# Kernel optimization log

Hardware: AMD Instinct MI355X
Metric: run time of the kernel (lower is better)

Reference implementation:

```python
import jax, jax.numpy as jnp
import numpy as np

N_NODES = 100000
N_EDGES = 3200000
IN_C, HID, OUT_C = 128, 256, 128
N_GRAPHS = 64
EPS = 1e-5


def setup_inputs() -> dict:
    key = jax.random.key(0)
    ks = jax.random.split(key, 16)
    x = jax.random.normal(ks[0], (N_NODES, IN_C), dtype=jnp.float32)
    edge_index = jax.random.randint(ks[1], (2, N_EDGES), 0, N_NODES, dtype=jnp.int64 if jax.config.jax_enable_x64 else jnp.int32)
    batch = jnp.sort(jax.random.randint(ks[2], (N_NODES,), 0, N_GRAPHS, dtype=jnp.int32))
    def glorot(k, shape):
        lim = jnp.sqrt(6.0 / (shape[-2] + shape[-1]))
        return jax.random.uniform(k, shape, jnp.float32, -lim, lim)
    return {
        "x": x,
        "W_in": glorot(ks[3], (IN_C, HID)),
        "b_in": jnp.zeros((HID,), jnp.float32),
        "g_in": jnp.ones((HID,), jnp.float32),
        "be_in": jnp.zeros((HID,), jnp.float32),
        "W_hid": glorot(ks[4], (2, HID, HID)),
        "b_hid": jnp.zeros((2, HID), jnp.float32),
        "g_hid": jnp.ones((2, HID), jnp.float32),
        "be_hid": jnp.zeros((2, HID), jnp.float32),
        "W_out": glorot(ks[5], (HID, OUT_C)),
        "b_out": jnp.zeros((OUT_C,), jnp.float32),
        "g_out": jnp.ones((OUT_C,), jnp.float32),
        "be_out": jnp.zeros((OUT_C,), jnp.float32),
        "edge_index": edge_index,
        "batch": batch,
    }


def _gcn_norm(edge_index, n_nodes):
    # add self-loops, symmetric deg^-1/2 normalization (PyG GCNConv defaults)
    loop = jnp.arange(n_nodes, dtype=edge_index.dtype)
    src = jnp.concatenate([edge_index[0], loop])
    dst = jnp.concatenate([edge_index[1], loop])
    deg = jax.ops.segment_sum(jnp.ones_like(dst, dtype=jnp.float32), dst, num_segments=n_nodes)
    dinv = jnp.where(deg > 0, jax.lax.rsqrt(deg), 0.0)
    norm = dinv[src] * dinv[dst]  # [E+N]
    return src, dst, norm


def _block(x, W, b, g, be, src, dst, norm, n_nodes):
    h = x @ W  # [N, out]
    agg = jax.ops.segment_sum(h[src] * norm[:, None], dst, num_segments=n_nodes) + b
    a = jax.nn.leaky_relu(agg, negative_slope=0.01)
    mu = jnp.mean(a, axis=0)
    var = jnp.mean(jnp.square(a - mu), axis=0)
    return (a - mu) * jax.lax.rsqrt(var + EPS) * g + be


def reference(x, W_in, b_in, g_in, be_in, W_hid, b_hid, g_hid, be_hid,
              W_out, b_out, g_out, be_out, edge_index, batch):
    n = x.shape[0]
    src, dst, norm = _gcn_norm(edge_index, n)
    h = _block(x, W_in, b_in, g_in, be_in, src, dst, norm, n)
    for i in range(W_hid.shape[0]):
        h = _block(h, W_hid[i], b_hid[i], g_hid[i], be_hid[i], src, dst, norm, n)
    h = _block(h, W_out, b_out, g_out, be_out, src, dst, norm, n)
    # global mean pool over graphs
    sums = jax.ops.segment_sum(h, batch, num_segments=N_GRAPHS)
    cnts = jax.ops.segment_sum(jnp.ones((n,), h.dtype), batch, num_segments=N_GRAPHS)
    return sums / jnp.maximum(cnts, 1.0)[:, None]
```

## Files before the change

### kernel.cpp

```cpp
#include <hip/hip_runtime.h>
#include <stdint.h>

#define EPS_LN 1e-5f

typedef short bf16x8 __attribute__((ext_vector_type(8)));
typedef float f32x4  __attribute__((ext_vector_type(4)));

__device__ __forceinline__ unsigned short f2bf(float f) {
    unsigned u = __float_as_uint(f);
    unsigned r = (u + 0x7fffu + ((u >> 16) & 1u)) >> 16;
    return (unsigned short)r;
}
__device__ __forceinline__ float bf_lo(unsigned u) { return __uint_as_float(u << 16); }
__device__ __forceinline__ float bf_hi(unsigned u) { return __uint_as_float(u & 0xffff0000u); }

__device__ __forceinline__ void async16(void* lds, const void* g) {
    __builtin_amdgcn_global_load_lds(
        (const __attribute__((address_space(1))) unsigned int*)g,
        (__attribute__((address_space(3))) unsigned int*)lds, 16, 0, 0);
}


__global__ void count_deg_kernel(const int* __restrict__ dst, int E, unsigned* __restrict__ deg) {
    int e = blockIdx.x * blockDim.x + threadIdx.x;
    if (e < E) atomicAdd(&deg[dst[e]], 1u);
}

__global__ void dinv_kernel(const unsigned* __restrict__ deg, float* __restrict__ dinv, int N) {
    int i = blockIdx.x * blockDim.x + threadIdx.x;
    if (i < N) dinv[i] = rsqrtf((float)(deg[i] + 1u));
}

__global__ void block_sums_kernel(const unsigned* __restrict__ deg, unsigned* __restrict__ part, int N) {
    __shared__ unsigned s[256];
    int t = threadIdx.x;
    int i0 = blockIdx.x * 512 + t * 2;
    unsigned a = (i0 < N) ? deg[i0] : 0u;
    unsigned b = (i0 + 1 < N) ? deg[i0 + 1] : 0u;
    s[t] = a + b;
    __syncthreads();
    for (int off = 128; off > 0; off >>= 1) {
        if (t < off) s[t] += s[t + off];
        __syncthreads();
    }
    if (t == 0) part[blockIdx.x] = s[0];
}

__global__ void scan_part_kernel(unsigned* __restrict__ part, unsigned* __restrict__ row_ptr,
                                 int NB, int N) {
    __shared__ unsigned s[256];
    int t = threadIdx.x;
    unsigned v = (t < NB) ? part[t] : 0u;
    s[t] = v;
    __syncthreads();
    for (int off = 1; off < 256; off <<= 1) {
        unsigned u = (t >= off) ? s[t - off] : 0u;
        __syncthreads();
        s[t] += u;
        __syncthreads();
    }
    if (t < NB) part[t] = s[t] - v;
    if (t == 255) row_ptr[N] = s[255];
}

__global__ void scan_blocks_kernel(const unsigned* __restrict__ deg, const unsigned* __restrict__ part,
                                   unsigned* __restrict__ row_ptr, unsigned* __restrict__ cursor, int N) {
    __shared__ unsigned s[256];
    int t = threadIdx.x;
    int i0 = blockIdx.x * 512 + t * 2;
    unsigned a = (i0 < N) ? deg[i0] : 0u;
    unsigned b = (i0 + 1 < N) ? deg[i0 + 1] : 0u;
    unsigned pair = a + b;
    s[t] = pair;
    __syncthreads();
    for (int off = 1; off < 256; off <<= 1) {
        unsigned u = (t >= off) ? s[t - off] : 0u;
        __syncthreads();
        s[t] += u;
        __syncthreads();
    }
    unsigned excl = s[t] - pair + part[blockIdx.x];
    if (i0 < N)     { row_ptr[i0] = excl;         cursor[i0] = excl; }
    if (i0 + 1 < N) { row_ptr[i0 + 1] = excl + a; cursor[i0 + 1] = excl + a; }
}

__global__ void fill_csr_kernel(const int* __restrict__ src, const int* __restrict__ dst,
                                const float* __restrict__ dinv, int E,
                                unsigned* __restrict__ cursor, uint2* __restrict__ csr) {
    int e = blockIdx.x * blockDim.x + threadIdx.x;
    if (e < E) {
        int d = dst[e];
        int s = src[e];
        unsigned pos = atomicAdd(&cursor[d], 1u);
        float w = dinv[d] * dinv[s];
        csr[pos] = make_uint2((unsigned)s, __float_as_uint(w));
    }
}

__global__ void cvt_bf_kernel(const float* __restrict__ in, unsigned* __restrict__ out, int n2) {
    int i = blockIdx.x * blockDim.x + threadIdx.x;
    if (i < n2) {
        float2 v = *reinterpret_cast<const float2*>(&in[(size_t)i * 2]);
        out[i] = (unsigned)f2bf(v.x) | ((unsigned)f2bf(v.y) << 16);
    }
}

__global__ void prep_wt_kernel(const float* __restrict__ W, unsigned short* __restrict__ Wt,
                               int K, int NN) {
    int idx = blockIdx.x * blockDim.x + threadIdx.x;
    if (idx < K * NN) {
        int k = idx / NN, c = idx % NN;
        Wt[(size_t)c * K + k] = f2bf(W[idx]);
    }
}

__global__ void prep_wout_kernel(const float* __restrict__ W, const float* __restrict__ s_arr,
                                 unsigned short* __restrict__ Wt) {
    int idx = blockIdx.x * blockDim.x + threadIdx.x;
    if (idx < 256 * 128) {
        int k = idx >> 7, c = idx & 127;
        Wt[(size_t)c * 256 + k] = f2bf(s_arr[k] * W[idx]);
    }
}

__global__ void tw_kernel(const float* __restrict__ W, const float* __restrict__ t_arr,
                          float* __restrict__ tW) {
    int c = threadIdx.x;
    float acc = 0.f;
    for (int k = 0; k < 256; ++k) acc += t_arr[k] * W[k * 128 + c];
    tW[c] = acc;
}

template<int VEC, bool AFF, bool FINAL>
__global__ void aggregate_bf(const unsigned* __restrict__ X, void* __restrict__ outp,
                             const unsigned* __restrict__ row_ptr, const uint2* __restrict__ csr,
                             const float* __restrict__ dinv,
                             const float* __restrict__ s_aff, const float* __restrict__ t_aff,
                             const float* __restrict__ tW, const float* __restrict__ bias, int N) {
    const unsigned RSU = VEC * 32;
    int node = blockIdx.x * 4 + (threadIdx.x >> 6);
    if (node >= N) return;
    node = __builtin_amdgcn_readfirstlane(node);
    int lane = threadIdx.x & 63;
    unsigned cu = (unsigned)lane * (VEC / 2);

    float di = dinv[node];
    float w0 = di * di;
    float acc[VEC];
    float wsum = w0;
    {
        const unsigned* xr = X + (size_t)((unsigned)node * RSU + cu);
        if constexpr (VEC == 4) {
            uint2 v = *reinterpret_cast<const uint2*>(xr);
            acc[0] = w0 * bf_lo(v.x); acc[1] = w0 * bf_hi(v.x);
            acc[2] = w0 * bf_lo(v.y); acc[3] = w0 * bf_hi(v.y);
        } else {
            unsigned v = *xr;
            acc[0] = w0 * bf_lo(v); acc[1] = w0 * bf_hi(v);
        }
    }
    unsigned e0 = __builtin_amdgcn_readfirstlane(row_ptr[node]);
    unsigned e1 = __builtin_amdgcn_readfirstlane(row_ptr[node + 1]);
    unsigned cnt = e1 - e0;
    unsigned full = cnt & ~7u;

    if constexpr (VEC == 4) {
        for (unsigned i = 0; i < full; i += 8) {
            uint2 p[8];
            #pragma unroll
            for (int u = 0; u < 8; ++u) p[u] = csr[e0 + i + u];
            uint2 v[8];
            #pragma unroll
            for (int u = 0; u < 8; ++u)
                v[u] = *reinterpret_cast<const uint2*>(X + (size_t)(p[u].x * RSU + cu));
            #pragma unroll
            for (int u = 0; u < 8; ++u) {
                float f = __uint_as_float(p[u].y);
                acc[0] += f * bf_lo(v[u].x); acc[1] += f * bf_hi(v[u].x);
                acc[2] += f * bf_lo(v[u].y); acc[3] += f * bf_hi(v[u].y);
                wsum += f;
            }
        }
        for (unsigned i = full; i < cnt; ++i) {
            uint2 p = csr[e0 + i];
            uint2 v = *reinterpret_cast<const uint2*>(X + (size_t)(p.x * RSU + cu));
            float f = __uint_as_float(p.y);
            acc[0] += f * bf_lo(v.x); acc[1] += f * bf_hi(v.x);
            acc[2] += f * bf_lo(v.y); acc[3] += f * bf_hi(v.y);
            wsum += f;
        }
    } else {
        for (unsigned i = 0; i < full; i += 8) {
            uint2 p[8];
            #pragma unroll
            for (int u = 0; u < 8; ++u) p[u] = csr[e0 + i + u];
            unsigned v[8];
            #pragma unroll
            for (int u = 0; u < 8; ++u) v[u] = X[(size_t)(p[u].x * RSU + cu)];
            #pragma unroll
            for (int u = 0; u < 8; ++u) {
                float f = __uint_as_float(p[u].y);
                acc[0] += f * bf_lo(v[u]); acc[1] += f * bf_hi(v[u]);
                wsum += f;
            }
        }
        for (unsigned i = full; i < cnt; ++i) {
            uint2 p = csr[e0 + i];
            unsigned v = X[(size_t)(p.x * RSU + cu)];
            float f = __uint_as_float(p.y);
            acc[0] += f * bf_lo(v); acc[1] += f * bf_hi(v);
            wsum += f;
        }
    }

    int col = lane * VEC;
    float z[VEC];
    #pragma unroll
    for (int j = 0; j < VEC; ++j) {
        float f = acc[j];
        if constexpr (AFF) f = s_aff[col + j] * f + t_aff[col + j] * wsum;
        if constexpr (FINAL) {
            f = f + wsum * tW[col + j] + bias[col + j];
            f = f > 0.f ? f : 0.01f * f;
        }
        z[j] = f;
    }
    if constexpr (FINAL) {
        float* of = (float*)outp;
        *reinterpret_cast<float2*>(&of[(size_t)node * (VEC * 64) + col]) = make_float2(z[0], z[1]);
    } else {
        unsigned* ou = (unsigned*)outp;
        if constexpr (VEC == 4) {
            uint2 p;
            p.x = (unsigned)f2bf(z[0]) | ((unsigned)f2bf(z[1]) << 16);
            p.y = (unsigned)f2bf(z[2]) | ((unsigned)f2bf(z[3]) << 16);
            *reinterpret_cast<uint2*>(&ou[(size_t)((unsigned)node * RSU + cu)]) = p;
        } else {
            ou[(size_t)((unsigned)node * RSU + cu)] = (unsigned)f2bf(z[0]) | ((unsigned)f2bf(z[1]) << 16);
        }
    }
}

template<int K, int NN, bool EPI>
__launch_bounds__(256)
__global__ void gemm_mfma(const unsigned short* __restrict__ Z, const unsigned short* __restrict__ Wt,
                          const float* __restrict__ bias, unsigned short* __restrict__ out,
                          float* __restrict__ stat_sum, float* __restrict__ stat_sq, int M) {
    __shared__ char smem[32768];
    __shared__ float csum[128], csq[128];

    const int tid = threadIdx.x;
    const int lane = tid & 63;
    const int w = tid >> 6;
    const int wr = (w >> 1) * 64;
    const int wc = (w & 1) * 64;
    const int rowBase = blockIdx.x * 128;
    const int colBase = blockIdx.y * 128;
    const int frow = lane & 15;
    const int kgrp = lane >> 4;

    f32x4 acc[4][4] = {};

    for (int kt = 0; kt < K / 64; ++kt) {
        #pragma unroll
        for (int i = 0; i < 4; ++i) {
            int g = (i * 4 + w) * 64 + lane;
            int r = g >> 3;
            int bl = (g & 7) * 16;
            int bg = bl ^ ((r & 7) << 4);
            const char* src = (const char*)Z + (((size_t)(rowBase + r) * K + kt * 64) << 1) + bg;
            async16(&smem[(i * 4 + w) * 1024], src);
        }
        #pragma unroll
        for (int i = 0; i < 4; ++i) {
            int g = (i * 4 + w) * 64 + lane;
            int r = g >> 3;
            int bl = (g & 7) * 16;
            int bg = bl ^ ((r & 7) << 4);
            const char* src = (const char*)Wt + (((size_t)(colBase + r) * K + kt * 64) << 1) + bg;
            async16(&smem[16384 + (i * 4 + w) * 1024], src);
        }
        __syncthreads();
        #pragma unroll
        for (int kk = 0; kk < 2; ++kk) {
            const int kbyte = kk * 64 + kgrp * 16;
            bf16x8 af[4], bfr[4];
            #pragma unroll
            for (int m = 0; m < 4; ++m) {
                int r = wr + m * 16 + frow;
                af[m] = *reinterpret_cast<const bf16x8*>(&smem[r * 128 + (kbyte ^ ((r & 7) << 4))]);
            }
            #pragma unroll
            for (int n = 0; n < 4; ++n) {
                int c = wc + n * 16 + frow;
                bfr[n] = *reinterpret_cast<const bf16x8*>(&smem[16384 + c * 128 + (kbyte ^ ((c & 7) << 4))]);
            }
            #pragma unroll
            for (int m = 0; m < 4; ++m)
                #pragma unroll
                for (int n = 0; n < 4; ++n)
                    acc[m][n] = __builtin_amdgcn_mfma_f32_16x16x32_bf16(bfr[n], af[m], acc[m][n], 0, 0, 0);
        }
        __syncthreads();
    }

    if constexpr (EPI) {
        if (tid < 128) { csum[tid] = 0.f; csq[tid] = 0.f; }
        __syncthreads();
    }

    #pragma unroll
    for (int n = 0; n < 4; ++n) {
        const int c_local = wc + n * 16 + kgrp * 4;
        const int col = colBase + c_local;
        float4 b4 = make_float4(0.f, 0.f, 0.f, 0.f);
        if constexpr (EPI) b4 = *reinterpret_cast<const float4*>(&bias[col]);
        float ps[4] = {0.f, 0.f, 0.f, 0.f}, pq[4] = {0.f, 0.f, 0.f, 0.f};
        #pragma unroll
        for (int m = 0; m < 4; ++m) {
            int row = rowBase + wr + m * 16 + frow;
            if (row < M) {
                float f0 = acc[m][n][0] + b4.x;
                float f1 = acc[m][n][1] + b4.y;
                float f2 = acc[m][n][2] + b4.z;
                float f3 = acc[m][n][3] + b4.w;
                if constexpr (EPI) {
                    f0 = f0 > 0.f ? f0 : 0.01f * f0;
                    f1 = f1 > 0.f ? f1 : 0.01f * f1;
                    f2 = f2 > 0.f ? f2 : 0.01f * f2;
                    f3 = f3 > 0.f ? f3 : 0.01f * f3;
                }
                uint2 pk;
                pk.x = (unsigned)f2bf(f0) | ((unsigned)f2bf(f1) << 16);
                pk.y = (unsigned)f2bf(f2) | ((unsigned)f2bf(f3) << 16);
                *reinterpret_cast<uint2*>(&out[(size_t)row * NN + col]) = pk;
                if constexpr (EPI) {
                    ps[0] += f0; ps[1] += f1; ps[2] += f2; ps[3] += f3;
                    pq[0] += f0 * f0; pq[1] += f1 * f1; pq[2] += f2 * f2; pq[3] += f3 * f3;
                }
            }
        }
        if constexpr (EPI) {
            #pragma unroll
            for (int s = 1; s < 16; s <<= 1) {
                #pragma unroll
                for (int j = 0; j < 4; ++j) {
                    ps[j] += __shfl_xor(ps[j], s);
                    pq[j] += __shfl_xor(pq[j], s);
                }
            }
            if (frow == 0) {
                #pragma unroll
                for (int j = 0; j < 4; ++j) {
                    atomicAdd(&csum[c_local + j], ps[j]);
                    atomicAdd(&csq[c_local + j], pq[j]);
                }
            }
        }
    }
    if constexpr (EPI) {
        __syncthreads();
        if (tid < 128) {
            atomicAdd(&stat_sum[colBase + tid], csum[tid]);
            atomicAdd(&stat_sq[colBase + tid], csq[tid]);
        }
    }
}

__global__ void finalize_kernel(const float* __restrict__ g, const float* __restrict__ be,
                                float* __restrict__ stat_sum, float* __restrict__ stat_sq,
                                float* __restrict__ s_arr, float* __restrict__ t_arr,
                                int C, float invN) {
    int i = threadIdx.x;
    if (i < C) {
        float mu = stat_sum[i] * invN;
        float var = stat_sq[i] * invN - mu * mu;
        float rs = rsqrtf(var + EPS_LN);
        float s = g[i] * rs;
        s_arr[i] = s;
        t_arr[i] = be[i] - mu * s;
        stat_sum[i] = 0.f;
        stat_sq[i] = 0.f;
    }
}

__global__ void stats_pool_kernel(const float* __restrict__ A, const int* __restrict__ batch,
                                  float* __restrict__ stat_sum, float* __restrict__ stat_sq,
                                  float* __restrict__ psums, float* __restrict__ pcnt, int N) {
    int c = threadIdx.x;
    int n0 = blockIdx.x * 256;
    if (n0 >= N) return;
    int n1 = min(n0 + 256, N);
    float cs = 0.f, cq = 0.f;
    float acc = 0.f, cacc = 0.f;
    int curg = -1;
    for (int n = n0; n < n1; ++n) {
        float v = A[(size_t)n * 128 + c];
        cs += v; cq += v * v;
        int g = batch[n];
        if (g != curg) {
            if (curg >= 0) {
                atomicAdd(&psums[curg * 128 + c], acc);
                if (c == 0) atomicAdd(&pcnt[curg], cacc);
            }
            acc = 0.f; cacc = 0.f; curg = g;
        }
        acc += v;
        cacc += 1.f;
    }
    if (curg >= 0) {
        atomicAdd(&psums[curg * 128 + c], acc);
        if (c == 0) atomicAdd(&pcnt[curg], cacc);
    }
    atomicAdd(&stat_sum[c], cs);
    atomicAdd(&stat_sq[c], cq);
}

__global__ void divide_kernel(const float* __restrict__ psums, const float* __restrict__ pcnt,
                              const float* __restrict__ s_arr, const float* __restrict__ t_arr,
                              float* __restrict__ out) {
    int i = blockIdx.x * blockDim.x + threadIdx.x;
    if (i < 64 * 128) {
        int g = i >> 7, c = i & 127;
        float cnt = pcnt[g];
        out[i] = (cnt > 0.f) ? s_arr[c] * (psums[i] / cnt) + t_arr[c] : 0.f;
    }
}

extern "C" void kernel_launch(void* const* d_in, const int* in_sizes, int n_in,
                              void* d_out, int out_size, void* d_ws, size_t ws_size,
                              hipStream_t stream) {
    const float* x      = (const float*)d_in[0];
    const float* W_in   = (const float*)d_in[1];
    const float* b_in   = (const float*)d_in[2];
    const float* g_in   = (const float*)d_in[3];
    const float* be_in  = (const float*)d_in[4];
    const float* W_hid  = (const float*)d_in[5];
    const float* b_hid  = (const float*)d_in[6];
    const float* g_hid  = (const float*)d_in[7];
    const float* be_hid = (const float*)d_in[8];
    const float* W_out  = (const float*)d_in[9];
    const float* b_out  = (const float*)d_in[10];
    const float* g_out  = (const float*)d_in[11];
    const float* be_out = (const float*)d_in[12];
    const int*   eidx   = (const int*)d_in[13];
    const int*   batch  = (const int*)d_in[14];
    float* out = (float*)d_out;

    const int N = in_sizes[14];
    const int E = in_sizes[13] / 2;
    const int Npad = ((N + 127) / 128) * 128;
    const int NB = (N + 511) / 512;
    const int* e_src = eidx;
    const int* e_dst = eidx + E;

    char* ws = (char*)d_ws;
    size_t off = 0;
    auto alloc = [&](size_t bytes) -> void* {
        void* p = ws + off;
        off = (off + bytes + 255) & ~(size_t)255;
        return p;
    };
    char* B1 = (char*)alloc((size_t)Npad * 256 * 2);
    char* B2 = (char*)alloc((size_t)Npad * 256 * 2);
    unsigned* deg      = (unsigned*)alloc((size_t)N * 4);
    float*    dinv     = (float*)alloc((size_t)N * 4);
    unsigned* row_ptr  = (unsigned*)alloc((size_t)(N + 1) * 4);
    unsigned* cursor   = (unsigned*)alloc((size_t)N * 4);
    unsigned* part     = (unsigned*)alloc(256 * 4);
    uint2*    csr      = (uint2*)alloc((size_t)E * 8);
    unsigned short* Wt_in  = (unsigned short*)alloc(256 * 128 * 2);
    unsigned short* Wt_h0  = (unsigned short*)alloc(256 * 256 * 2);
    unsigned short* Wt_h1  = (unsigned short*)alloc(256 * 256 * 2);
    unsigned short* Wt_out = (unsigned short*)alloc(128 * 256 * 2);
    float*    tW       = (float*)alloc(128 * 4);
    float*    stat_sum = (float*)alloc(256 * 4);
    float*    stat_sq  = (float*)alloc(256 * 4);
    float*    s_arr    = (float*)alloc(256 * 4);
    float*    t_arr    = (float*)alloc(256 * 4);
    float*    psums    = (float*)alloc(64 * 128 * 4);
    float*    pcnt     = (float*)alloc(64 * 4);

    const float invN = 1.0f / (float)N;

    hipMemsetAsync(deg, 0, (size_t)N * 4, stream);
    hipMemsetAsync(stat_sum, 0, 256 * 4, stream);
    hipMemsetAsync(stat_sq, 0, 256 * 4, stream);
    hipMemsetAsync(psums, 0, 64 * 128 * 4, stream);
    hipMemsetAsync(pcnt, 0, 64 * 4, stream);

    int egrid = (E + 255) / 256;
    count_deg_kernel<<<egrid, 256, 0, stream>>>(e_dst, E, deg);
    dinv_kernel<<<(N + 255) / 256, 256, 0, stream>>>(deg, dinv, N);
    block_sums_kernel<<<NB, 256, 0, stream>>>(deg, part, N);
    scan_part_kernel<<<1, 256, 0, stream>>>(part, row_ptr, NB, N);
    scan_blocks_kernel<<<NB, 256, 0, stream>>>(deg, part, row_ptr, cursor, N);
    fill_csr_kernel<<<egrid, 256, 0, stream>>>(e_src, e_dst, dinv, E, cursor, csr);

    cvt_bf_kernel<<<(N * 64 + 255) / 256, 256, 0, stream>>>(x, (unsigned*)B2, N * 64);
    prep_wt_kernel<<<(128 * 256 + 255) / 256, 256, 0, stream>>>(W_in, Wt_in, 128, 256);
    prep_wt_kernel<<<(256 * 256 + 255) / 256, 256, 0, stream>>>(W_hid, Wt_h0, 256, 256);
    prep_wt_kernel<<<(256 * 256 + 255) / 256, 256, 0, stream>>>(W_hid + 65536, Wt_h1, 256, 256);

    const int aggGrid = (N + 3) / 4;
    dim3 gg256(Npad / 128, 2);
    dim3 gg128(Npad / 128, 1);

    aggregate_bf<2, false, false><<<aggGrid, 256, 0, stream>>>(
        (const unsigned*)B2, B1, row_ptr, csr, dinv, nullptr, nullptr, nullptr, nullptr, N);
    gemm_mfma<128, 256, true><<<gg256, 256, 0, stream>>>(
        (const unsigned short*)B1, Wt_in, b_in, (unsigned short*)B2, stat_sum, stat_sq, N);
    finalize_kernel<<<1, 256, 0, stream>>>(g_in, be_in, stat_sum, stat_sq, s_arr, t_arr, 256, invN);

    aggregate_bf<4, true, false><<<aggGrid, 256, 0, stream>>>(
        (const unsigned*)B2, B1, row_ptr, csr, dinv, s_arr, t_arr, nullptr, nullptr, N);
    gemm_mfma<256, 256, true><<<gg256, 256, 0, stream>>>(
        (const unsigned short*)B1, Wt_h0, b_hid, (unsigned short*)B2, stat_sum, stat_sq, N);
    finalize_kernel<<<1, 256, 0, stream>>>(g_hid, be_hid, stat_sum, stat_sq, s_arr, t_arr, 256, invN);

    aggregate_bf<4, true, false><<<aggGrid, 256, 0, stream>>>(
        (const unsigned*)B2, B1, row_ptr, csr, dinv, s_arr, t_arr, nullptr, nullptr, N);
    gemm_mfma<256, 256, true><<<gg256, 256, 0, stream>>>(
        (const unsigned short*)B1, Wt_h1, b_hid + 256, (unsigned short*)B2, stat_sum, stat_sq, N);
    finalize_kernel<<<1, 256, 0, stream>>>(g_hid + 256, be_hid + 256, stat_sum, stat_sq, s_arr, t_arr, 256, invN);

    prep_wout_kernel<<<(256 * 128 + 255) / 256, 256, 0, stream>>>(W_out, s_arr, Wt_out);
    tw_kernel<<<1, 128, 0, stream>>>(W_out, t_arr, tW);
    gemm_mfma<256, 128, false><<<gg128, 256, 0, stream>>>(
        (const unsigned short*)B2, Wt_out, nullptr, (unsigned short*)B1, nullptr, nullptr, N);
    aggregate_bf<2, false, true><<<aggGrid, 256, 0, stream>>>(
        (const unsigned*)B1, B2, row_ptr, csr, dinv, nullptr, nullptr, tW, b_out, N);

    stats_pool_kernel<<<(N + 255) / 256, 128, 0, stream>>>(
        (const float*)B2, batch, stat_sum, stat_sq, psums, pcnt, N);
    finalize_kernel<<<1, 256, 0, stream>>>(g_out, be_out, stat_sum, stat_sq, s_arr, t_arr, 128, invN);
    divide_kernel<<<(64 * 128 + 255) / 256, 256, 0, stream>>>(psums, pcnt, s_arr, t_arr, out);
}
```

Measured before the change: 1.292 ms.

## Fuse neighbor aggregation with MFMA GEMM and BN stats per layer

Adds a fused kernel where each wave aggregates 16 nodes' neighbor rows into registers, applies the affine BN transform, stores the bf16 rows to LDS, and multiplies them by the weight matrix with MFMA. Bias, leaky-relu and statistics accumulation happen in the epilogue. This removes the intermediate aggregated buffer round-trip and separate launches for the first three layers. Each node is now handled by 4 lanes with a serial edge loop, which gives less unrolled gather parallelism than the previous per-node wave design. Unused VEC=4 paths in the aggregate kernel are removed.

```diff
diff --git a/kernel.cpp b/kernel.cpp
--- a/kernel.cpp
+++ b/kernel.cpp
@@ -131,6 +131,179 @@
     tW[c] = acc;
 }
 
+template<int K, int NN, bool AFF>
+__launch_bounds__(256)
+__global__ void fused_layer(const unsigned* __restrict__ in, const unsigned short* __restrict__ Wt,
+                            const float* __restrict__ bias,
+                            const float* __restrict__ s_aff, const float* __restrict__ t_aff,
+                            unsigned short* __restrict__ out,
+                            const unsigned* __restrict__ row_ptr, const uint2* __restrict__ csr,
+                            const float* __restrict__ dinv,
+                            float* __restrict__ stat_sum, float* __restrict__ stat_sq, int N) {
+    constexpr int COLS = K / 4;
+    constexpr int NU   = K / 8;
+    constexpr int NL4  = NU / 4;
+    constexpr int NF   = NN / 16;
+
+    __shared__ char alds[4 * 16 * K * 2];
+    __shared__ float csum[NN], csq[NN];
+
+    const int tid = threadIdx.x;
+    const int lane = tid & 63;
+    const int w = tid >> 6;
+
+    for (int i = tid; i < NN; i += 256) { csum[i] = 0.f; csq[i] = 0.f; }
+    __syncthreads();
+
+    const int nq = lane >> 2;
+    const int part = lane & 3;
+    const int rowBase = blockIdx.x * 64 + w * 16;
+    const int node = rowBase + nq;
+
+    float acc[COLS];
+    #pragma unroll
+    for (int i = 0; i < COLS; ++i) acc[i] = 0.f;
+    float wsum = 0.f;
+    unsigned e0 = 0, e1 = 0;
+
+    if (node < N) {
+        float di = dinv[node];
+        float w0 = di * di;
+        const unsigned* bp = in + (size_t)node * (K / 2) + part * NU;
+        uint4 v[NL4];
+        #pragma unroll
+        for (int i = 0; i < NL4; ++i) v[i] = *reinterpret_cast<const uint4*>(bp + i * 4);
+        #pragma unroll
+        for (int i = 0; i < NL4; ++i) {
+            unsigned uu[4] = {v[i].x, v[i].y, v[i].z, v[i].w};
+            #pragma unroll
+            for (int q = 0; q < 4; ++q) {
+                acc[i * 8 + q * 2 + 0] = w0 * bf_lo(uu[q]);
+                acc[i * 8 + q * 2 + 1] = w0 * bf_hi(uu[q]);
+            }
+        }
+        wsum = w0;
+        e0 = row_ptr[node];
+        e1 = row_ptr[node + 1];
+    }
+
+    for (unsigned e = e0; e < e1; ++e) {
+        uint2 p = csr[e];
+        float f = __uint_as_float(p.y);
+        const unsigned* bp = in + (size_t)p.x * (K / 2) + part * NU;
+        uint4 v[NL4];
+        #pragma unroll
+        for (int i = 0; i < NL4; ++i) v[i] = *reinterpret_cast<const uint4*>(bp + i * 4);
+        #pragma unroll
+        for (int i = 0; i < NL4; ++i) {
+            unsigned uu[4] = {v[i].x, v[i].y, v[i].z, v[i].w};
+            #pragma unroll
+            for (int q = 0; q < 4; ++q) {
+                acc[i * 8 + q * 2 + 0] += f * bf_lo(uu[q]);
+                acc[i * 8 + q * 2 + 1] += f * bf_hi(uu[q]);
+            }
+        }
+        wsum += f;
+    }
+
+    if constexpr (AFF) {
+        #pragma unroll
+        for (int i = 0; i < COLS / 4; ++i) {
+            int c = part * COLS + i * 4;
+            float4 s4 = *reinterpret_cast<const float4*>(&s_aff[c]);
+            float4 t4 = *reinterpret_cast<const float4*>(&t_aff[c]);
+            acc[i * 4 + 0] = s4.x * acc[i * 4 + 0] + t4.x * wsum;
+            acc[i * 4 + 1] = s4.y * acc[i * 4 + 1] + t4.y * wsum;
+            acc[i * 4 + 2] = s4.z * acc[i * 4 + 2] + t4.z * wsum;
+            acc[i * 4 + 3] = s4.w * acc[i * 4 + 3] + t4.w * wsum;
+        }
+    }
+
+    {
+        char* myrow = alds + w * (16 * K * 2) + nq * (K * 2);
+        #pragma unroll
+        for (int i = 0; i < NL4; ++i) {
+            uint4 pk;
+            pk.x = (unsigned)f2bf(acc[i * 8 + 0]) | ((unsigned)f2bf(acc[i * 8 + 1]) << 16);
+            pk.y = (unsigned)f2bf(acc[i * 8 + 2]) | ((unsigned)f2bf(acc[i * 8 + 3]) << 16);
+            pk.z = (unsigned)f2bf(acc[i * 8 + 4]) | ((unsigned)f2bf(acc[i * 8 + 5]) << 16);
+            pk.w = (unsigned)f2bf(acc[i * 8 + 6]) | ((unsigned)f2bf(acc[i * 8 + 7]) << 16);
+            int off = (part * (NU * 4) + i * 16) ^ ((nq & 7) << 4);
+            *reinterpret_cast<uint4*>(myrow + off) = pk;
+        }
+    }
+
+    const int frow = lane & 15;
+    const int kgrp = lane >> 4;
+    f32x4 macc[NF] = {};
+    const char* wbase = alds + w * (16 * K * 2);
+
+    #pragma unroll
+    for (int kt = 0; kt < K / 32; ++kt) {
+        int aoff = frow * (K * 2) + ((kt * 64 + kgrp * 16) ^ ((frow & 7) << 4));
+        bf16x8 af = *reinterpret_cast<const bf16x8*>(wbase + aoff);
+        #pragma unroll
+        for (int g = 0; g < NF / 4; ++g) {
+            bf16x8 bf0 = *reinterpret_cast<const bf16x8*>(Wt + ((size_t)((g * 4 + 0) * 16 + frow)) * K + kt * 32 + kgrp * 8);
+            bf16x8 bf1 = *reinterpret_cast<const bf16x8*>(Wt + ((size_t)((g * 4 + 1) * 16 + frow)) * K + kt * 32 + kgrp * 8);
+            bf16x8 bf2 = *reinterpret_cast<const bf16x8*>(Wt + ((size_t)((g * 4 + 2) * 16 + frow)) * K + kt * 32 + kgrp * 8);
+            bf16x8 bf3 = *reinterpret_cast<const bf16x8*>(Wt + ((size_t)((g * 4 + 3) * 16 + frow)) * K + kt * 32 + kgrp * 8);
+            macc[g * 4 + 0] = __builtin_amdgcn_mfma_f32_16x16x32_bf16(bf0, af, macc[g * 4 + 0], 0, 0, 0);
+            macc[g * 4 + 1] = __builtin_amdgcn_mfma_f32_16x16x32_bf16(bf1, af, macc[g * 4 + 1], 0, 0, 0);
+            macc[g * 4 + 2] = __builtin_amdgcn_mfma_f32_16x16x32_bf16(bf2, af, macc[g * 4 + 2], 0, 0, 0);
+            macc[g * 4 + 3] = __builtin_amdgcn_mfma_f32_16x16x32_bf16(bf3, af, macc[g * 4 + 3], 0, 0, 0);
+        }
+    }
+
+    const int orow = rowBase + frow;
+    const bool rok = orow < N;
+    #pragma unroll
+    for (int n = 0; n < NF; ++n) {
+        const int c0 = n * 16 + kgrp * 4;
+        float4 b4 = *reinterpret_cast<const float4*>(&bias[c0]);
+        float f0 = macc[n][0] + b4.x;
+        float f1 = macc[n][1] + b4.y;
+        float f2 = macc[n][2] + b4.z;
+        float f3 = macc[n][3] + b4.w;
+        f0 = f0 > 0.f ? f0 : 0.01f * f0;
+        f1 = f1 > 0.f ? f1 : 0.01f * f1;
+        f2 = f2 > 0.f ? f2 : 0.01f * f2;
+        f3 = f3 > 0.f ? f3 : 0.01f * f3;
+        float ps[4], pq[4];
+        if (rok) {
+            uint2 pk;
+            pk.x = (unsigned)f2bf(f0) | ((unsigned)f2bf(f1) << 16);
+            pk.y = (unsigned)f2bf(f2) | ((unsigned)f2bf(f3) << 16);
+            *reinterpret_cast<uint2*>(&out[(size_t)orow * NN + c0]) = pk;
+            ps[0] = f0; ps[1] = f1; ps[2] = f2; ps[3] = f3;
+            pq[0] = f0 * f0; pq[1] = f1 * f1; pq[2] = f2 * f2; pq[3] = f3 * f3;
+        } else {
+            ps[0] = ps[1] = ps[2] = ps[3] = 0.f;
+            pq[0] = pq[1] = pq[2] = pq[3] = 0.f;
+        }
+        #pragma unroll
+        for (int s = 1; s < 16; s <<= 1) {
+            #pragma unroll
+            for (int j = 0; j < 4; ++j) {
+                ps[j] += __shfl_xor(ps[j], s);
+                pq[j] += __shfl_xor(pq[j], s);
+            }
+        }
+        if (frow == 0) {
+            #pragma unroll
+            for (int j = 0; j < 4; ++j) {
+                atomicAdd(&csum[c0 + j], ps[j]);
+                atomicAdd(&csq[c0 + j], pq[j]);
+            }
+        }
+    }
+    __syncthreads();
+    for (int i = tid; i < NN; i += 256) {
+        atomicAdd(&stat_sum[i], csum[i]);
+        atomicAdd(&stat_sq[i], csq[i]);
+    }
+}
+
 template<int VEC, bool AFF, bool FINAL>
 __global__ void aggregate_bf(const unsigned* __restrict__ X, void* __restrict__ outp,
                              const unsigned* __restrict__ row_ptr, const uint2* __restrict__ csr,
@@ -150,67 +323,34 @@
     float wsum = w0;
     {
         const unsigned* xr = X + (size_t)((unsigned)node * RSU + cu);
-        if constexpr (VEC == 4) {
-            uint2 v = *reinterpret_cast<const uint2*>(xr);
-            acc[0] = w0 * bf_lo(v.x); acc[1] = w0 * bf_hi(v.x);
-            acc[2] = w0 * bf_lo(v.y); acc[3] = w0 * bf_hi(v.y);
-        } else {
-            unsigned v = *xr;
-            acc[0] = w0 * bf_lo(v); acc[1] = w0 * bf_hi(v);
-        }
+        unsigned v = *xr;
+        acc[0] = w0 * bf_lo(v); acc[1] = w0 * bf_hi(v);
     }
     unsigned e0 = __builtin_amdgcn_readfirstlane(row_ptr[node]);
     unsigned e1 = __builtin_amdgcn_readfirstlane(row_ptr[node + 1]);
     unsigned cnt = e1 - e0;
     unsigned full = cnt & ~7u;
 
-    if constexpr (VEC == 4) {
-        for (unsigned i = 0; i < full; i += 8) {
-            uint2 p[8];
-            #pragma unroll
-            for (int u = 0; u < 8; ++u) p[u] = csr[e0 + i + u];
-            uint2 v[8];
-            #pragma unroll
-            for (int u = 0; u < 8; ++u)
-                v[u] = *reinterpret_cast<const uint2*>(X + (size_t)(p[u].x * RSU + cu));
-            #pragma unroll
-            for (int u = 0; u < 8; ++u) {
-                float f = __uint_as_float(p[u].y);
-                acc[0] += f * bf_lo(v[u].x); acc[1] += f * bf_hi(v[u].x);
-                acc[2] += f * bf_lo(v[u].y); acc[3] += f * bf_hi(v[u].y);
-                wsum += f;
-            }
-        }
-        for (unsigned i = full; i < cnt; ++i) {
-            uint2 p = csr[e0 + i];
-            uint2 v = *reinterpret_cast<const uint2*>(X + (size_t)(p.x * RSU + cu));
-            float f = __uint_as_float(p.y);
-            acc[0] += f * bf_lo(v.x); acc[1] += f * bf_hi(v.x);
-            acc[2] += f * bf_lo(v.y); acc[3] += f * bf_hi(v.y);
+    for (unsigned i = 0; i < full; i += 8) {
+        uint2 p[8];
+        #pragma unroll
+        for (int u = 0; u < 8; ++u) p[u] = csr[e0 + i + u];
+        unsigned v[8];
+        #pragma unroll
+        for (int u = 0; u < 8; ++u) v[u] = X[(size_t)(p[u].x * RSU + cu)];
+        #pragma unroll
+        for (int u = 0; u < 8; ++u) {
+            float f = __uint_as_float(p[u].y);
+            acc[0] += f * bf_lo(v[u]); acc[1] += f * bf_hi(v[u]);
             wsum += f;
         }
-    } else {
-        for (unsigned i = 0; i < full; i += 8) {
-            uint2 p[8];
-            #pragma unroll
-            for (int u = 0; u < 8; ++u) p[u] = csr[e0 + i + u];
-            unsigned v[8];
-            #pragma unroll
-            for (int u = 0; u < 8; ++u) v[u] = X[(size_t)(p[u].x * RSU + cu)];
-            #pragma unroll
-            for (int u = 0; u < 8; ++u) {
-                float f = __uint_as_float(p[u].y);
-                acc[0] += f * bf_lo(v[u]); acc[1] += f * bf_hi(v[u]);
-                wsum += f;
-            }
-        }
-        for (unsigned i = full; i < cnt; ++i) {
-            uint2 p = csr[e0 + i];
-            unsigned v = X[(size_t)(p.x * RSU + cu)];
-            float f = __uint_as_float(p.y);
-            acc[0] += f * bf_lo(v); acc[1] += f * bf_hi(v);
-            wsum += f;
-        }
+    }
+    for (unsigned i = full; i < cnt; ++i) {
+        uint2 p = csr[e0 + i];
+        unsigned v = X[(size_t)(p.x * RSU + cu)];
+        float f = __uint_as_float(p.y);
+        acc[0] += f * bf_lo(v); acc[1] += f * bf_hi(v);
+        wsum += f;
     }
 
     int col = lane * VEC;
@@ -230,14 +370,7 @@
         *reinterpret_cast<float2*>(&of[(size_t)node * (VEC * 64) + col]) = make_float2(z[0], z[1]);
     } else {
         unsigned* ou = (unsigned*)outp;
-        if constexpr (VEC == 4) {
-            uint2 p;
-            p.x = (unsigned)f2bf(z[0]) | ((unsigned)f2bf(z[1]) << 16);
-            p.y = (unsigned)f2bf(z[2]) | ((unsigned)f2bf(z[3]) << 16);
-            *reinterpret_cast<uint2*>(&ou[(size_t)((unsigned)node * RSU + cu)]) = p;
-        } else {
-            ou[(size_t)((unsigned)node * RSU + cu)] = (unsigned)f2bf(z[0]) | ((unsigned)f2bf(z[1]) << 16);
-        }
+        ou[(size_t)((unsigned)node * RSU + cu)] = (unsigned)f2bf(z[0]) | ((unsigned)f2bf(z[1]) << 16);
     }
 }
 
@@ -502,37 +635,32 @@
     prep_wt_kernel<<<(256 * 256 + 255) / 256, 256, 0, stream>>>(W_hid, Wt_h0, 256, 256);
     prep_wt_kernel<<<(256 * 256 + 255) / 256, 256, 0, stream>>>(W_hid + 65536, Wt_h1, 256, 256);
 
-    const int aggGrid = (N + 3) / 4;
-    dim3 gg256(Npad / 128, 2);
-    dim3 gg128(Npad / 128, 1);
-
-    aggregate_bf<2, false, false><<<aggGrid, 256, 0, stream>>>(
-        (const unsigned*)B2, B1, row_ptr, csr, dinv, nullptr, nullptr, nullptr, nullptr, N);
-    gemm_mfma<128, 256, true><<<gg256, 256, 0, stream>>>(
-        (const unsigned short*)B1, Wt_in, b_in, (unsigned short*)B2, stat_sum, stat_sq, N);
+    const int fusedGrid = (N + 63) / 64;
+
+    fused_layer<128, 256, false><<<fusedGrid, 256, 0, stream>>>(
+        (const unsigned*)B2, Wt_in, b_in, nullptr, nullptr, (unsigned short*)B1,
+        row_ptr, csr, dinv, stat_sum, stat_sq, N);
     finalize_kernel<<<1, 256, 0, stream>>>(g_in, be_in, stat_sum, stat_sq, s_arr, t_arr, 256, invN);
 
-    aggregate_bf<4, true, false><<<aggGrid, 256, 0, stream>>>(
-        (const unsigned*)B2, B1, row_ptr, csr, dinv, s_arr, t_arr, nullptr, nullptr, N);
-    gemm_mfma<256, 256, true><<<gg256, 256, 0, stream>>>(
-        (const unsigned short*)B1, Wt_h0, b_hid, (unsigned short*)B2, stat_sum, stat_sq, N);
+    fused_layer<256, 256, true><<<fusedGrid, 256, 0, stream>>>(
+        (const unsigned*)B1, Wt_h0, b_hid, s_arr, t_arr, (unsigned short*)B2,
+        row_ptr, csr, dinv, stat_sum, stat_sq, N);
     finalize_kernel<<<1, 256, 0, stream>>>(g_hid, be_hid, stat_sum, stat_sq, s_arr, t_arr, 256, invN);
 
-    aggregate_bf<4, true, false><<<aggGrid, 256, 0, stream>>>(
-        (const unsigned*)B2, B1, row_ptr, csr, dinv, s_arr, t_arr, nullptr, nullptr, N);
-    gemm_mfma<256, 256, true><<<gg256, 256, 0, stream>>>(
-        (const unsigned short*)B1, Wt_h1, b_hid + 256, (unsigned short*)B2, stat_sum, stat_sq, N);
+    fused_layer<256, 256, true><<<fusedGrid, 256, 0, stream>>>(
+        (const unsigned*)B2, Wt_h1, b_hid + 256, s_arr, t_arr, (unsigned short*)B1,
+        row_ptr, csr, dinv, stat_sum, stat_sq, N);
     finalize_kernel<<<1, 256, 0, stream>>>(g_hid + 256, be_hid + 256, stat_sum, stat_sq, s_arr, t_arr, 256, invN);
 
     prep_wout_kernel<<<(256 * 128 + 255) / 256, 256, 0, stream>>>(W_out, s_arr, Wt_out);
     tw_kernel<<<1, 128, 0, stream>>>(W_out, t_arr, tW);
-    gemm_mfma<256, 128, false><<<gg128, 256, 0, stream>>>(
-        (const unsigned short*)B2, Wt_out, nullptr, (unsigned short*)B1, nullptr, nullptr, N);
-    aggregate_bf<2, false, true><<<aggGrid, 256, 0, stream>>>(
-        (const unsigned*)B1, B2, row_ptr, csr, dinv, nullptr, nullptr, tW, b_out, N);
+    gemm_mfma<256, 128, false><<<dim3(Npad / 128, 1), 256, 0, stream>>>(
+        (const unsigned short*)B1, Wt_out, nullptr, (unsigned short*)B2, nullptr, nullptr, N);
+    aggregate_bf<2, false, true><<<(N + 3) / 4, 256, 0, stream>>>(
+        (const unsigned*)B2, B1, row_ptr, csr, dinv, nullptr, nullptr, tW, b_out, N);
 
     stats_pool_kernel<<<(N + 255) / 256, 128, 0, stream>>>(
-        (const float*)B2, batch, stat_sum, stat_sq, psums, pcnt, N);
+        (const float*)B1, batch, stat_sum, stat_sq, psums, pcnt, N);
     finalize_kernel<<<1, 256, 0, stream>>>(g_out, be_out, stat_sum, stat_sq, s_arr, t_arr, 128, invN);
     divide_kernel<<<(64 * 128 + 255) / 256, 256, 0, stream>>>(psums, pcnt, s_arr, t_arr, out);
 }
```

Result: slower. 1.718 ms (+33.0%).

## Fuse prep and finalize kernels, use half-wave per node in aggregation

Applied to the files above, without the earlier changes.

Folds the dinv computation into the scan kernel and merges the x/weight conversion kernels into one launch. The per-layer finalize kernels are removed by recomputing the batch-norm scale and shift inside the consumers (aggregate, W_out prep, divide), with a separate stats buffer per layer so no re-zeroing is needed. Aggregation now assigns 32 lanes per node with wider 16-byte gathers instead of 64 lanes with 8-byte gathers. This cuts launch count and serial tiny kernels, in exchange for some redundant per-block rsqrt work and different gather granularity.

```diff
diff --git a/kernel.cpp b/kernel.cpp
--- a/kernel.cpp
+++ b/kernel.cpp
@@ -24,11 +24,6 @@
 __global__ void count_deg_kernel(const int* __restrict__ dst, int E, unsigned* __restrict__ deg) {
     int e = blockIdx.x * blockDim.x + threadIdx.x;
     if (e < E) atomicAdd(&deg[dst[e]], 1u);
-}
-
-__global__ void dinv_kernel(const unsigned* __restrict__ deg, float* __restrict__ dinv, int N) {
-    int i = blockIdx.x * blockDim.x + threadIdx.x;
-    if (i < N) dinv[i] = rsqrtf((float)(deg[i] + 1u));
 }
 
 __global__ void block_sums_kernel(const unsigned* __restrict__ deg, unsigned* __restrict__ part, int N) {
@@ -64,7 +59,8 @@
 }
 
 __global__ void scan_blocks_kernel(const unsigned* __restrict__ deg, const unsigned* __restrict__ part,
-                                   unsigned* __restrict__ row_ptr, unsigned* __restrict__ cursor, int N) {
+                                   unsigned* __restrict__ row_ptr, unsigned* __restrict__ cursor,
+                                   float* __restrict__ dinv, int N) {
     __shared__ unsigned s[256];
     int t = threadIdx.x;
     int i0 = blockIdx.x * 512 + t * 2;
@@ -80,8 +76,14 @@
         __syncthreads();
     }
     unsigned excl = s[t] - pair + part[blockIdx.x];
-    if (i0 < N)     { row_ptr[i0] = excl;         cursor[i0] = excl; }
-    if (i0 + 1 < N) { row_ptr[i0 + 1] = excl + a; cursor[i0 + 1] = excl + a; }
+    if (i0 < N) {
+        row_ptr[i0] = excl; cursor[i0] = excl;
+        dinv[i0] = rsqrtf((float)(a + 1u));
+    }
+    if (i0 + 1 < N) {
+        row_ptr[i0 + 1] = excl + a; cursor[i0 + 1] = excl + a;
+        dinv[i0 + 1] = rsqrtf((float)(b + 1u));
+    }
 }
 
 __global__ void fill_csr_kernel(const int* __restrict__ src, const int* __restrict__ dst,
@@ -97,78 +99,105 @@
     }
 }
 
-__global__ void cvt_bf_kernel(const float* __restrict__ in, unsigned* __restrict__ out, int n2) {
+__global__ void prep_all_kernel(const float* __restrict__ x, unsigned* __restrict__ xbf,
+                                const float* __restrict__ W_in, unsigned short* __restrict__ Wt_in,
+                                const float* __restrict__ W_hid, unsigned short* __restrict__ Wt_h0,
+                                unsigned short* __restrict__ Wt_h1, int n2) {
     int i = blockIdx.x * blockDim.x + threadIdx.x;
     if (i < n2) {
-        float2 v = *reinterpret_cast<const float2*>(&in[(size_t)i * 2]);
-        out[i] = (unsigned)f2bf(v.x) | ((unsigned)f2bf(v.y) << 16);
-    }
-}
-
-__global__ void prep_wt_kernel(const float* __restrict__ W, unsigned short* __restrict__ Wt,
-                               int K, int NN) {
-    int idx = blockIdx.x * blockDim.x + threadIdx.x;
-    if (idx < K * NN) {
-        int k = idx / NN, c = idx % NN;
-        Wt[(size_t)c * K + k] = f2bf(W[idx]);
-    }
-}
-
-__global__ void prep_wout_kernel(const float* __restrict__ W, const float* __restrict__ s_arr,
-                                 unsigned short* __restrict__ Wt) {
-    int idx = blockIdx.x * blockDim.x + threadIdx.x;
-    if (idx < 256 * 128) {
-        int k = idx >> 7, c = idx & 127;
-        Wt[(size_t)c * 256 + k] = f2bf(s_arr[k] * W[idx]);
-    }
-}
-
-__global__ void tw_kernel(const float* __restrict__ W, const float* __restrict__ t_arr,
-                          float* __restrict__ tW) {
-    int c = threadIdx.x;
-    float acc = 0.f;
-    for (int k = 0; k < 256; ++k) acc += t_arr[k] * W[k * 128 + c];
-    tW[c] = acc;
-}
-
-template<int VEC, bool AFF, bool FINAL>
+        float2 v = *reinterpret_cast<const float2*>(&x[(size_t)i * 2]);
+        xbf[i] = (unsigned)f2bf(v.x) | ((unsigned)f2bf(v.y) << 16);
+        return;
+    }
+    int r = i - n2;
+    if (r < 32768) {
+        int k = r >> 8, c = r & 255;
+        Wt_in[(size_t)c * 128 + k] = f2bf(W_in[r]);
+    } else if (r < 32768 + 65536) {
+        r -= 32768;
+        int k = r >> 8, c = r & 255;
+        Wt_h0[(size_t)c * 256 + k] = f2bf(W_hid[r]);
+    } else if (r < 32768 + 131072) {
+        r -= 32768 + 65536;
+        int k = r >> 8, c = r & 255;
+        Wt_h1[(size_t)c * 256 + k] = f2bf(W_hid[65536 + r]);
+    }
+}
+
+template<int UPL, bool AFF, bool FINAL>
 __global__ void aggregate_bf(const unsigned* __restrict__ X, void* __restrict__ outp,
                              const unsigned* __restrict__ row_ptr, const uint2* __restrict__ csr,
                              const float* __restrict__ dinv,
-                             const float* __restrict__ s_aff, const float* __restrict__ t_aff,
+                             const float* __restrict__ ssum, const float* __restrict__ ssq,
+                             const float* __restrict__ gg, const float* __restrict__ be, float invN,
                              const float* __restrict__ tW, const float* __restrict__ bias, int N) {
-    const unsigned RSU = VEC * 32;
-    int node = blockIdx.x * 4 + (threadIdx.x >> 6);
+    constexpr int C = UPL * 64;
+    constexpr unsigned RSU = C / 2;
+    constexpr int PC = UPL * 2;
+
+    __shared__ float sL[AFF ? C : 1], tL[AFF ? C : 1];
+    if constexpr (AFF) {
+        for (int i = threadIdx.x; i < C; i += 256) {
+            float mu = ssum[i] * invN;
+            float var = ssq[i] * invN - mu * mu;
+            float s = gg[i] * rsqrtf(var + EPS_LN);
+            sL[i] = s;
+            tL[i] = be[i] - mu * s;
+        }
+        __syncthreads();
+    }
+
+    int node = blockIdx.x * 8 + (threadIdx.x >> 5);
     if (node >= N) return;
-    node = __builtin_amdgcn_readfirstlane(node);
-    int lane = threadIdx.x & 63;
-    unsigned cu = (unsigned)lane * (VEC / 2);
+    int ll = threadIdx.x & 31;
+    unsigned cu = (unsigned)ll * UPL;
 
     float di = dinv[node];
     float w0 = di * di;
-    float acc[VEC];
+    float acc[PC];
     float wsum = w0;
     {
         const unsigned* xr = X + (size_t)((unsigned)node * RSU + cu);
-        if constexpr (VEC == 4) {
+        if constexpr (UPL == 4) {
+            uint4 v = *reinterpret_cast<const uint4*>(xr);
+            unsigned uu[4] = {v.x, v.y, v.z, v.w};
+            #pragma unroll
+            for (int q = 0; q < 4; ++q) {
+                acc[q * 2 + 0] = w0 * bf_lo(uu[q]);
+                acc[q * 2 + 1] = w0 * bf_hi(uu[q]);
+            }
+        } else {
             uint2 v = *reinterpret_cast<const uint2*>(xr);
             acc[0] = w0 * bf_lo(v.x); acc[1] = w0 * bf_hi(v.x);
             acc[2] = w0 * bf_lo(v.y); acc[3] = w0 * bf_hi(v.y);
-        } else {
-            unsigned v = *xr;
-            acc[0] = w0 * bf_lo(v); acc[1] = w0 * bf_hi(v);
-        }
-    }
-    unsigned e0 = __builtin_amdgcn_readfirstlane(row_ptr[node]);
-    unsigned e1 = __builtin_amdgcn_readfirstlane(row_ptr[node + 1]);
+        }
+    }
+    unsigned e0 = row_ptr[node];
+    unsigned e1 = row_ptr[node + 1];
     unsigned cnt = e1 - e0;
     unsigned full = cnt & ~7u;
 
-    if constexpr (VEC == 4) {
-        for (unsigned i = 0; i < full; i += 8) {
-            uint2 p[8];
-            #pragma unroll
-            for (int u = 0; u < 8; ++u) p[u] = csr[e0 + i + u];
+    for (unsigned i = 0; i < full; i += 8) {
+        uint2 p[8];
+        #pragma unroll
+        for (int u = 0; u < 8; ++u) p[u] = csr[e0 + i + u];
+        if constexpr (UPL == 4) {
+            uint4 v[8];
+            #pragma unroll
+            for (int u = 0; u < 8; ++u)
+                v[u] = *reinterpret_cast<const uint4*>(X + (size_t)(p[u].x * RSU + cu));
+            #pragma unroll
+            for (int u = 0; u < 8; ++u) {
+                float f = __uint_as_float(p[u].y);
+                unsigned uu[4] = {v[u].x, v[u].y, v[u].z, v[u].w};
+                #pragma unroll
+                for (int q = 0; q < 4; ++q) {
+                    acc[q * 2 + 0] += f * bf_lo(uu[q]);
+                    acc[q * 2 + 1] += f * bf_hi(uu[q]);
+                }
+                wsum += f;
+            }
+        } else {
             uint2 v[8];
             #pragma unroll
             for (int u = 0; u < 8; ++u)
@@ -181,44 +210,32 @@
                 wsum += f;
             }
         }
-        for (unsigned i = full; i < cnt; ++i) {
-            uint2 p = csr[e0 + i];
+    }
+    for (unsigned i = full; i < cnt; ++i) {
+        uint2 p = csr[e0 + i];
+        float f = __uint_as_float(p.y);
+        if constexpr (UPL == 4) {
+            uint4 v = *reinterpret_cast<const uint4*>(X + (size_t)(p.x * RSU + cu));
+            unsigned uu[4] = {v.x, v.y, v.z, v.w};
+            #pragma unroll
+            for (int q = 0; q < 4; ++q) {
+                acc[q * 2 + 0] += f * bf_lo(uu[q]);
+                acc[q * 2 + 1] += f * bf_hi(uu[q]);
+            }
+        } else {
             uint2 v = *reinterpret_cast<const uint2*>(X + (size_t)(p.x * RSU + cu));
-            float f = __uint_as_float(p.y);
             acc[0] += f * bf_lo(v.x); acc[1] += f * bf_hi(v.x);
             acc[2] += f * bf_lo(v.y); acc[3] += f * bf_hi(v.y);
-            wsum += f;
-        }
-    } else {
-        for (unsigned i = 0; i < full; i += 8) {
-            uint2 p[8];
-            #pragma unroll
-            for (int u = 0; u < 8; ++u) p[u] = csr[e0 + i + u];
-            unsigned v[8];
-            #pragma unroll
-            for (int u = 0; u < 8; ++u) v[u] = X[(size_t)(p[u].x * RSU + cu)];
-            #pragma unroll
-            for (int u = 0; u < 8; ++u) {
-                float f = __uint_as_float(p[u].y);
-                acc[0] += f * bf_lo(v[u]); acc[1] += f * bf_hi(v[u]);
-                wsum += f;
-            }
-        }
-        for (unsigned i = full; i < cnt; ++i) {
-            uint2 p = csr[e0 + i];
-            unsigned v = X[(size_t)(p.x * RSU + cu)];
-            float f = __uint_as_float(p.y);
-            acc[0] += f * bf_lo(v); acc[1] += f * bf_hi(v);
-            wsum += f;
-        }
-    }
-
-    int col = lane * VEC;
-    float z[VEC];
+        }
+        wsum += f;
+    }
+
+    int col = ll * PC;
+    float z[PC];
     #pragma unroll
-    for (int j = 0; j < VEC; ++j) {
+    for (int j = 0; j < PC; ++j) {
         float f = acc[j];
-        if constexpr (AFF) f = s_aff[col + j] * f + t_aff[col + j] * wsum;
+        if constexpr (AFF) f = sL[col + j] * f + tL[col + j] * wsum;
         if constexpr (FINAL) {
             f = f + wsum * tW[col + j] + bias[col + j];
             f = f > 0.f ? f : 0.01f * f;
@@ -227,16 +244,21 @@
     }
     if constexpr (FINAL) {
         float* of = (float*)outp;
-        *reinterpret_cast<float2*>(&of[(size_t)node * (VEC * 64) + col]) = make_float2(z[0], z[1]);
+        *reinterpret_cast<float4*>(&of[(size_t)node * C + col]) = make_float4(z[0], z[1], z[2], z[3]);
     } else {
         unsigned* ou = (unsigned*)outp;
-        if constexpr (VEC == 4) {
-            uint2 p;
-            p.x = (unsigned)f2bf(z[0]) | ((unsigned)f2bf(z[1]) << 16);
-            p.y = (unsigned)f2bf(z[2]) | ((unsigned)f2bf(z[3]) << 16);
-            *reinterpret_cast<uint2*>(&ou[(size_t)((unsigned)node * RSU + cu)]) = p;
+        if constexpr (UPL == 4) {
+            uint4 pk;
+            pk.x = (unsigned)f2bf(z[0]) | ((unsigned)f2bf(z[1]) << 16);
+            pk.y = (unsigned)f2bf(z[2]) | ((unsigned)f2bf(z[3]) << 16);
+            pk.z = (unsigned)f2bf(z[4]) | ((unsigned)f2bf(z[5]) << 16);
+            pk.w = (unsigned)f2bf(z[6]) | ((unsigned)f2bf(z[7]) << 16);
+            *reinterpret_cast<uint4*>(&ou[(size_t)((unsigned)node * RSU + cu)]) = pk;
         } else {
-            ou[(size_t)((unsigned)node * RSU + cu)] = (unsigned)f2bf(z[0]) | ((unsigned)f2bf(z[1]) << 16);
+            uint2 pk;
+            pk.x = (unsigned)f2bf(z[0]) | ((unsigned)f2bf(z[1]) << 16);
+            pk.y = (unsigned)f2bf(z[2]) | ((unsigned)f2bf(z[3]) << 16);
+            *reinterpret_cast<uint2*>(&ou[(size_t)((unsigned)node * RSU + cu)]) = pk;
         }
     }
 }
@@ -367,20 +389,30 @@
     }
 }
 
-__global__ void finalize_kernel(const float* __restrict__ g, const float* __restrict__ be,
-                                float* __restrict__ stat_sum, float* __restrict__ stat_sq,
-                                float* __restrict__ s_arr, float* __restrict__ t_arr,
-                                int C, float invN) {
-    int i = threadIdx.x;
-    if (i < C) {
-        float mu = stat_sum[i] * invN;
-        float var = stat_sq[i] * invN - mu * mu;
-        float rs = rsqrtf(var + EPS_LN);
-        float s = g[i] * rs;
-        s_arr[i] = s;
-        t_arr[i] = be[i] - mu * s;
-        stat_sum[i] = 0.f;
-        stat_sq[i] = 0.f;
+__global__ void prep_wout_tw(const float* __restrict__ W,
+                             const float* __restrict__ ssum, const float* __restrict__ ssq,
+                             const float* __restrict__ gg, const float* __restrict__ be, float invN,
+                             unsigned short* __restrict__ Wt, float* __restrict__ tW) {
+    if (blockIdx.x < 128) {
+        int idx = blockIdx.x * 256 + threadIdx.x;
+        int k = idx >> 7, c = idx & 127;
+        float mu = ssum[k] * invN;
+        float var = ssq[k] * invN - mu * mu;
+        float s = gg[k] * rsqrtf(var + EPS_LN);
+        Wt[(size_t)c * 256 + k] = f2bf(s * W[idx]);
+    } else {
+        int c = threadIdx.x;
+        if (c < 128) {
+            float acc = 0.f;
+            for (int k = 0; k < 256; ++k) {
+                float mu = ssum[k] * invN;
+                float var = ssq[k] * invN - mu * mu;
+                float s = gg[k] * rsqrtf(var + EPS_LN);
+                float t = be[k] - mu * s;
+                acc += t * W[k * 128 + c];
+            }
+            tW[c] = acc;
+        }
     }
 }
 
@@ -417,13 +449,18 @@
 }
 
 __global__ void divide_kernel(const float* __restrict__ psums, const float* __restrict__ pcnt,
-                              const float* __restrict__ s_arr, const float* __restrict__ t_arr,
+                              const float* __restrict__ ssum, const float* __restrict__ ssq,
+                              const float* __restrict__ gg, const float* __restrict__ be, float invN,
                               float* __restrict__ out) {
     int i = blockIdx.x * blockDim.x + threadIdx.x;
     if (i < 64 * 128) {
         int g = i >> 7, c = i & 127;
+        float mu = ssum[c] * invN;
+        float var = ssq[c] * invN - mu * mu;
+        float s = gg[c] * rsqrtf(var + EPS_LN);
+        float t = be[c] - mu * s;
         float cnt = pcnt[g];
-        out[i] = (cnt > 0.f) ? s_arr[c] * (psums[i] / cnt) + t_arr[c] : 0.f;
+        out[i] = (cnt > 0.f) ? s * (psums[i] / cnt) + t : 0.f;
     }
 }
 
@@ -474,65 +511,63 @@
     unsigned short* Wt_h1  = (unsigned short*)alloc(256 * 256 * 2);
     unsigned short* Wt_out = (unsigned short*)alloc(128 * 256 * 2);
     float*    tW       = (float*)alloc(128 * 4);
-    float*    stat_sum = (float*)alloc(256 * 4);
-    float*    stat_sq  = (float*)alloc(256 * 4);
-    float*    s_arr    = (float*)alloc(256 * 4);
-    float*    t_arr    = (float*)alloc(256 * 4);
+    float*    stats    = (float*)alloc(4 * 512 * 4);
     float*    psums    = (float*)alloc(64 * 128 * 4);
     float*    pcnt     = (float*)alloc(64 * 4);
 
+    float* s1 = stats + 0 * 512, *q1 = s1 + 256;
+    float* s2 = stats + 1 * 512, *q2 = s2 + 256;
+    float* s3 = stats + 2 * 512, *q3 = s3 + 256;
+    float* s4 = stats + 3 * 512, *q4 = s4 + 256;
+
     const float invN = 1.0f / (float)N;
 
     hipMemsetAsync(deg, 0, (size_t)N * 4, stream);
-    hipMemsetAsync(stat_sum, 0, 256 * 4, stream);
-    hipMemsetAsync(stat_sq, 0, 256 * 4, stream);
-    hipMemsetAsync(psums, 0, 64 * 128 * 4, stream);
-    hipMemsetAsync(pcnt, 0, 64 * 4, stream);
+    hipMemsetAsync(stats, 0, ((char*)pcnt + 64 * 4) - (char*)stats, stream);
 
     int egrid = (E + 255) / 256;
     count_deg_kernel<<<egrid, 256, 0, stream>>>(e_dst, E, deg);
-    dinv_kernel<<<(N + 255) / 256, 256, 0, stream>>>(deg, dinv, N);
     block_sums_kernel<<<NB, 256, 0, stream>>>(deg, part, N);
     scan_part_kernel<<<1, 256, 0, stream>>>(part, row_ptr, NB, N);
-    scan_blocks_kernel<<<NB, 256, 0, stream>>>(deg, part, row_ptr, cursor, N);
+    scan_blocks_kernel<<<NB, 256, 0, stream>>>(deg, part, row_ptr, cursor, dinv, N);
     fill_csr_kernel<<<egrid, 256, 0, stream>>>(e_src, e_dst, dinv, E, cursor, csr);
 
-    cvt_bf_kernel<<<(N * 64 + 255) / 256, 256, 0, stream>>>(x, (unsigned*)B2, N * 64);
-    prep_wt_kernel<<<(128 * 256 + 255) / 256, 256, 0, stream>>>(W_in, Wt_in, 128, 256);
-    prep_wt_kernel<<<(256 * 256 + 255) / 256, 256, 0, stream>>>(W_hid, Wt_h0, 256, 256);
-    prep_wt_kernel<<<(256 * 256 + 255) / 256, 256, 0, stream>>>(W_hid + 65536, Wt_h1, 256, 256);
-
-    const int aggGrid = (N + 3) / 4;
+    {
+        int total = N * 64 + 32768 + 65536 + 65536;
+        prep_all_kernel<<<(total + 255) / 256, 256, 0, stream>>>(
+            x, (unsigned*)B2, W_in, Wt_in, W_hid, Wt_h0, Wt_h1, N * 64);
+    }
+
+    const int aggGrid = (N + 7) / 8;
     dim3 gg256(Npad / 128, 2);
-    dim3 gg128(Npad / 128, 1);
 
     aggregate_bf<2, false, false><<<aggGrid, 256, 0, stream>>>(
-        (const unsigned*)B2, B1, row_ptr, csr, dinv, nullptr, nullptr, nullptr, nullptr, N);
+        (const unsigned*)B2, B1, row_ptr, csr, dinv,
+        nullptr, nullptr, nullptr, nullptr, invN, nullptr, nullptr, N);
     gemm_mfma<128, 256, true><<<gg256, 256, 0, stream>>>(
-        (const unsigned short*)B1, Wt_in, b_in, (unsigned short*)B2, stat_sum, stat_sq, N);
-    finalize_kernel<<<1, 256, 0, stream>>>(g_in, be_in, stat_sum, stat_sq, s_arr, t_arr, 256, invN);
+        (const unsigned short*)B1, Wt_in, b_in, (unsigned short*)B2, s1, q1, N);
 
     aggregate_bf<4, true, false><<<aggGrid, 256, 0, stream>>>(
-        (const unsigned*)B2, B1, row_ptr, csr, dinv, s_arr, t_arr, nullptr, nullptr, N);
+        (const unsigned*)B2, B1, row_ptr, csr, dinv,
+        s1, q1, g_in, be_in, invN, nullptr, nullptr, N);
     gemm_mfma<256, 256, true><<<gg256, 256, 0, stream>>>(
-        (const unsigned short*)B1, Wt_h0, b_hid, (unsigned short*)B2, stat_sum, stat_sq, N);
-    finalize_kernel<<<1, 256, 0, stream>>>(g_hid, be_hid, stat_sum, stat_sq, s_arr, t_arr, 256, invN);
+        (const unsigned short*)B1, Wt_h0, b_hid, (unsigned short*)B2, s2, q2, N);
 
     aggregate_bf<4, true, false><<<aggGrid, 256, 0, stream>>>(
-        (const unsigned*)B2, B1, row_ptr, csr, dinv, s_arr, t_arr, nullptr, nullptr, N);
+        (const unsigned*)B2, B1, row_ptr, csr, dinv,
+        s2, q2, g_hid, be_hid, invN, nullptr, nullptr, N);
     gemm_mfma<256, 256, true><<<gg256, 256, 0, stream>>>(
-        (const unsigned short*)B1, Wt_h1, b_hid + 256, (unsigned short*)B2, stat_sum, stat_sq, N);
-    finalize_kernel<<<1, 256, 0, stream>>>(g_hid + 256, be_hid + 256, stat_sum, stat_sq, s_arr, t_arr, 256, invN);
-
-    prep_wout_kernel<<<(256 * 128 + 255) / 256, 256, 0, stream>>>(W_out, s_arr, Wt_out);
-    tw_kernel<<<1, 128, 0, stream>>>(W_out, t_arr, tW);
-    gemm_mfma<256, 128, false><<<gg128, 256, 0, stream>>>(
+        (const unsigned short*)B1, Wt_h1, b_hid + 256, (unsigned short*)B2, s3, q3, N);
+
+    prep_wout_tw<<<129, 256, 0, stream>>>(W_out, s3, q3, g_hid + 256, be_hid + 256, invN, Wt_out, tW);
+    gemm_mfma<256, 128, false><<<dim3(Npad / 128, 1), 256, 0, stream>>>(
         (const unsigned short*)B2, Wt_out, nullptr, (unsigned short*)B1, nullptr, nullptr, N);
     aggregate_bf<2, false, true><<<aggGrid, 256, 0, stream>>>(
-        (const unsigned*)B1, B2, row_ptr, csr, dinv, nullptr, nullptr, tW, b_out, N);
+        (const unsigned*)B1, B2, row_ptr, csr, dinv,
+        nullptr, nullptr, nullptr, nullptr, invN, tW, b_out, N);
 
     stats_pool_kernel<<<(N + 255) / 256, 128, 0, stream>>>(
-        (const float*)B2, batch, stat_sum, stat_sq, psums, pcnt, N);
-    finalize_kernel<<<1, 256, 0, stream>>>(g_out, be_out, stat_sum, stat_sq, s_arr, t_arr, 128, invN);
-    divide_kernel<<<(64 * 128 + 255) / 256, 256, 0, stream>>>(psums, pcnt, s_arr, t_arr, out);
-}
+        (const float*)B2, batch, s4, q4, psums, pcnt, N);
+    divide_kernel<<<(64 * 128 + 255) / 256, 256, 0, stream>>>(
+        psums, pcnt, s4, q4, g_out, be_out, invN, out);
+}
```

New measurement: 1.314 ms. No clear change (+1.7%).
